# Optimization experiments

Measured on AMD Instinct MI355X. Metric: run time of the kernel, lower is better.

Reference implementation:

```python
import jax, jax.numpy as jnp
import numpy as np


def setup_inputs() -> dict:
    key = jax.random.key(0)
    b, l, d_model, n_head, topk = 2, 2048, 1024, 16, 32
    dh = d_model // n_head
    k0, k1, k2, k3, k4 = jax.random.split(key, 5)
    s = 1.0 / np.sqrt(d_model)
    return {
        "q_in": jax.random.normal(k0, (b, l, d_model), jnp.float32),
        "kv_in": jax.random.normal(k1, (b, l, d_model), jnp.float32),
        "w_q": jax.random.normal(k2, (d_model, d_model), jnp.float32) * s,
        "w_kv": jax.random.normal(k3, (d_model, 2 * dh), jnp.float32) * s,
        "w_concat": jax.random.normal(k4, (d_model, d_model), jnp.float32) * s,
        "topk": topk,
        "n_head": n_head,
    }


def _l2norm_seq(x):
    # F.normalize default dim=1 -> normalize along the sequence axis (faithful to source)
    n = jnp.sqrt(jnp.sum(x * x, axis=1, keepdims=True))
    return x / jnp.maximum(n, 1e-12)


def reference(q_in, kv_in, w_q, w_kv, w_concat, topk, n_head):
    b, l, d_model = q_in.shape
    dh = d_model // n_head
    scale = 1.0 / np.sqrt(dh)

    q = q_in @ w_q                                  # (b, l, d_model)
    kv = kv_in @ w_kv                               # (b, l, 2*dh)
    k, v = kv[..., :dh], kv[..., dh:]
    k, v = _l2norm_seq(k), _l2norm_seq(v)           # (b, l, dh) single shared KV head

    q = q.reshape(b, l, n_head, dh).transpose(0, 2, 1, 3)  # (b, h, l, dh)

    # one similarity matrix reused for local attention and kNN retrieval
    sims = jnp.einsum('bhld,bmd->bhlm', q, k)       # (b, h, l, m)

    # local SDPA (KV head broadcast over query heads)
    local = jnp.einsum('bhlm,bmd->bhld', jax.nn.softmax(sims * scale, axis=-1), v)

    # exact inner-product kNN over stored keys (faiss memory stores k only,
    # so retrieved key == retrieved value == nearest stored key vectors)
    _, idx = jax.lax.top_k(sims, topk)              # (b, h, l, topk)
    mem = jax.vmap(lambda kk, ii: kk[ii])(k, idx)   # (b, h, l, topk, dh)

    s_ret = jnp.einsum('bhld,bhltd->bhlt', q, mem) * scale
    retrieved = jnp.einsum('bhlt,bhltd->bhld', jax.nn.softmax(s_ret, axis=-1), mem)

    out = (local + retrieved).transpose(0, 2, 1, 3).reshape(b, l, d_model)
    return out @ w_concat
```

## Files before the change

kernel.cpp:

```cpp
#include <hip/hip_runtime.h>
#include <cstddef>
#include <cstring>

#define B_    2
#define L_    2048
#define DM_   1024
#define NH_   16
#define DH_   64
#define SCALE_ 0.125f

typedef __bf16 bf16x8 __attribute__((ext_vector_type(8)));
typedef float  f32x4  __attribute__((ext_vector_type(4)));
typedef unsigned short ushort8v __attribute__((ext_vector_type(8)));
typedef unsigned short ushort4v __attribute__((ext_vector_type(4)));
typedef unsigned long long u64;
typedef unsigned int u32;

__device__ __forceinline__ u32 flipf(float f) {
    u32 u = __float_as_uint(f);
    return (u & 0x80000000u) ? ~u : (u | 0x80000000u);
}
__device__ __forceinline__ float bf2f(unsigned short u) {
    return __uint_as_float(((u32)u) << 16);
}
__device__ __forceinline__ unsigned short f2bf(float f) {
    __bf16 h = (__bf16)f;
    unsigned short u;
    __builtin_memcpy(&u, &h, 2);
    return u;
}
__device__ __forceinline__ u32 flip16(unsigned short u) {
    return (u & 0x8000u) ? (u32)(~u & 0xffffu) : (u32)(u | 0x8000u);
}
__device__ __forceinline__ unsigned short unflip16(u32 k) {
    return (k & 0x8000u) ? (unsigned short)(k ^ 0x8000u) : (unsigned short)(~k & 0xffffu);
}

__global__ __launch_bounds__(256)
void wsplit3(const float* __restrict__ W, unsigned short* __restrict__ w1,
             unsigned short* __restrict__ w2, unsigned short* __restrict__ w3,
             int K, int N) {
    const int n0 = blockIdx.x << 6;
    const int k0 = blockIdx.y << 6;
    const int t  = threadIdx.x;
    __shared__ float s[64][65];
    const int rr = t >> 4;
    const int c4 = (t & 15) << 2;
    #pragma unroll
    for (int rep = 0; rep < 4; ++rep) {
        int k = rr + (rep << 4);
        float4 x = *(const float4*)(W + (size_t)(k0 + k) * N + n0 + c4);
        s[k][c4+0] = x.x; s[k][c4+1] = x.y; s[k][c4+2] = x.z; s[k][c4+3] = x.w;
    }
    __syncthreads();
    #pragma unroll
    for (int rep = 0; rep < 4; ++rep) {
        int n = rr + (rep << 4);
        ushort4v h, m, l;
        #pragma unroll
        for (int j = 0; j < 4; ++j) {
            float x = s[c4 + j][n];
            unsigned short hh = f2bf(x);
            float r = x - bf2f(hh);
            unsigned short mm = f2bf(r);
            float r2 = r - bf2f(mm);
            h[j] = hh; m[j] = mm; l[j] = f2bf(r2);
        }
        size_t o = (size_t)(n0 + n) * K + k0 + c4;
        *(ushort4v*)(w1 + o) = h;
        *(ushort4v*)(w2 + o) = m;
        *(ushort4v*)(w3 + o) = l;
    }
}

__global__ __launch_bounds__(256)
void asplit3(const float* __restrict__ X, unsigned short* __restrict__ p1,
             unsigned short* __restrict__ p2, unsigned short* __restrict__ p3) {
    const size_t i = ((size_t)blockIdx.x * 256 + threadIdx.x) * 8;
    float4 x0 = *(const float4*)(X + i);
    float4 x1 = *(const float4*)(X + i + 4);
    float xv[8] = {x0.x, x0.y, x0.z, x0.w, x1.x, x1.y, x1.z, x1.w};
    ushort8v h, m, l;
    #pragma unroll
    for (int e = 0; e < 8; ++e) {
        float x = xv[e];
        unsigned short hh = f2bf(x);
        float r = x - bf2f(hh);
        unsigned short mm = f2bf(r);
        h[e] = hh; m[e] = mm; l[e] = f2bf(r - bf2f(mm));
    }
    *(ushort8v*)(p1 + i) = h;
    *(ushort8v*)(p2 + i) = m;
    *(ushort8v*)(p3 + i) = l;
}

__global__ __launch_bounds__(256)
void asplit2(const float* __restrict__ X, unsigned short* __restrict__ p1,
             unsigned short* __restrict__ p2) {
    const size_t i = ((size_t)blockIdx.x * 256 + threadIdx.x) * 8;
    float4 x0 = *(const float4*)(X + i);
    float4 x1 = *(const float4*)(X + i + 4);
    float xv[8] = {x0.x, x0.y, x0.z, x0.w, x1.x, x1.y, x1.z, x1.w};
    ushort8v h, l;
    #pragma unroll
    for (int e = 0; e < 8; ++e) {
        float x = xv[e];
        unsigned short hh = f2bf(x);
        h[e] = hh; l[e] = f2bf(x - bf2f(hh));
    }
    *(ushort8v*)(p1 + i) = h;
    *(ushort8v*)(p2 + i) = l;
}

__global__ __launch_bounds__(256)
void gemm6p(const unsigned short* __restrict__ a1, const unsigned short* __restrict__ a2,
            const unsigned short* __restrict__ a3,
            const unsigned short* __restrict__ w1, const unsigned short* __restrict__ w2,
            const unsigned short* __restrict__ w3,
            float* __restrict__ C, int N, int K) {
    __shared__ __align__(16) unsigned short sA[3][128][40];
    __shared__ __align__(16) unsigned short sW[3][64][40];
    const int t    = threadIdx.x;
    const int wv   = t >> 6;
    const int lane = t & 63;
    const int quad = lane >> 4;
    const int n15  = lane & 15;
    const int bm = blockIdx.y << 7;
    const int bn = blockIdx.x << 6;
    const int wm = (wv >> 1) << 6;
    const int wn = (wv & 1) << 5;
    f32x4 acc[4][2];
    #pragma unroll
    for (int i = 0; i < 4; ++i)
        #pragma unroll
        for (int j = 0; j < 2; ++j)
            #pragma unroll
            for (int r = 0; r < 4; ++r) acc[i][j][r] = 0.f;

    const int ar  = t >> 1,  acg = (t & 1) << 4;
    const int wr  = t >> 2,  wcg = (t & 3) << 3;
    const size_t ao = (size_t)(bm + ar) * K + acg;
    const size_t wo = (size_t)(bn + wr) * K + wcg;

    for (int k0 = 0; k0 < K; k0 += 32) {
        ushort8v A1a = *(const ushort8v*)(a1 + ao + k0);
        ushort8v A1b = *(const ushort8v*)(a1 + ao + k0 + 8);
        ushort8v A2a = *(const ushort8v*)(a2 + ao + k0);
        ushort8v A2b = *(const ushort8v*)(a2 + ao + k0 + 8);
        ushort8v A3a = *(const ushort8v*)(a3 + ao + k0);
        ushort8v A3b = *(const ushort8v*)(a3 + ao + k0 + 8);
        ushort8v u1 = *(const ushort8v*)(w1 + wo + k0);
        ushort8v u2 = *(const ushort8v*)(w2 + wo + k0);
        ushort8v u3 = *(const ushort8v*)(w3 + wo + k0);
        __syncthreads();
        *(ushort8v*)&sA[0][ar][acg]     = A1a;
        *(ushort8v*)&sA[0][ar][acg + 8] = A1b;
        *(ushort8v*)&sA[1][ar][acg]     = A2a;
        *(ushort8v*)&sA[1][ar][acg + 8] = A2b;
        *(ushort8v*)&sA[2][ar][acg]     = A3a;
        *(ushort8v*)&sA[2][ar][acg + 8] = A3b;
        *(ushort8v*)&sW[0][wr][wcg] = u1;
        *(ushort8v*)&sW[1][wr][wcg] = u2;
        *(ushort8v*)&sW[2][wr][wcg] = u3;
        __syncthreads();
        bf16x8 af[3][4];
        #pragma unroll
        for (int mi = 0; mi < 4; ++mi) {
            af[0][mi] = *(const bf16x8*)&sA[0][wm + (mi << 4) + n15][quad << 3];
            af[1][mi] = *(const bf16x8*)&sA[1][wm + (mi << 4) + n15][quad << 3];
            af[2][mi] = *(const bf16x8*)&sA[2][wm + (mi << 4) + n15][quad << 3];
        }
        #pragma unroll
        for (int nj = 0; nj < 2; ++nj) {
            bf16x8 wf1 = *(const bf16x8*)&sW[0][wn + (nj << 4) + n15][quad << 3];
            bf16x8 wf2 = *(const bf16x8*)&sW[1][wn + (nj << 4) + n15][quad << 3];
            bf16x8 wf3 = *(const bf16x8*)&sW[2][wn + (nj << 4) + n15][quad << 3];
            #pragma unroll
            for (int mi = 0; mi < 4; ++mi) {
                acc[mi][nj] = __builtin_amdgcn_mfma_f32_16x16x32_bf16(af[0][mi], wf1, acc[mi][nj], 0, 0, 0);
                acc[mi][nj] = __builtin_amdgcn_mfma_f32_16x16x32_bf16(af[0][mi], wf2, acc[mi][nj], 0, 0, 0);
                acc[mi][nj] = __builtin_amdgcn_mfma_f32_16x16x32_bf16(af[1][mi], wf1, acc[mi][nj], 0, 0, 0);
                acc[mi][nj] = __builtin_amdgcn_mfma_f32_16x16x32_bf16(af[1][mi], wf2, acc[mi][nj], 0, 0, 0);
                acc[mi][nj] = __builtin_amdgcn_mfma_f32_16x16x32_bf16(af[0][mi], wf3, acc[mi][nj], 0, 0, 0);
                acc[mi][nj] = __builtin_amdgcn_mfma_f32_16x16x32_bf16(af[2][mi], wf1, acc[mi][nj], 0, 0, 0);
            }
        }
    }
    #pragma unroll
    for (int mi = 0; mi < 4; ++mi)
        #pragma unroll
        for (int nj = 0; nj < 2; ++nj)
            #pragma unroll
            for (int r = 0; r < 4; ++r)
                C[(size_t)(bm + wm + (mi << 4) + (quad << 2) + r) * N
                  + bn + wn + (nj << 4) + n15] = acc[mi][nj][r];
}

__global__ __launch_bounds__(256)
void gemm3p(const unsigned short* __restrict__ a1, const unsigned short* __restrict__ a2,
            const unsigned short* __restrict__ w1, const unsigned short* __restrict__ w2,
            float* __restrict__ C, int N, int K) {
    __shared__ __align__(16) unsigned short sA[2][128][40];
    __shared__ __align__(16) unsigned short sW[2][64][40];
    const int t    = threadIdx.x;
    const int wv   = t >> 6;
    const int lane = t & 63;
    const int quad = lane >> 4;
    const int n15  = lane & 15;
    const int bm = blockIdx.y << 7;
    const int bn = blockIdx.x << 6;
    const int wm = (wv >> 1) << 6;
    const int wn = (wv & 1) << 5;
    f32x4 acc[4][2];
    #pragma unroll
    for (int i = 0; i < 4; ++i)
        #pragma unroll
        for (int j = 0; j < 2; ++j)
            #pragma unroll
            for (int r = 0; r < 4; ++r) acc[i][j][r] = 0.f;

    const int ar  = t >> 1,  acg = (t & 1) << 4;
    const int wr  = t >> 2,  wcg = (t & 3) << 3;
    const size_t ao = (size_t)(bm + ar) * K + acg;
    const size_t wo = (size_t)(bn + wr) * K + wcg;

    for (int k0 = 0; k0 < K; k0 += 32) {
        ushort8v A1a = *(const ushort8v*)(a1 + ao + k0);
        ushort8v A1b = *(const ushort8v*)(a1 + ao + k0 + 8);
        ushort8v A2a = *(const ushort8v*)(a2 + ao + k0);
        ushort8v A2b = *(const ushort8v*)(a2 + ao + k0 + 8);
        ushort8v u1 = *(const ushort8v*)(w1 + wo + k0);
        ushort8v u2 = *(const ushort8v*)(w2 + wo + k0);
        __syncthreads();
        *(ushort8v*)&sA[0][ar][acg]     = A1a;
        *(ushort8v*)&sA[0][ar][acg + 8] = A1b;
        *(ushort8v*)&sA[1][ar][acg]     = A2a;
        *(ushort8v*)&sA[1][ar][acg + 8] = A2b;
        *(ushort8v*)&sW[0][wr][wcg] = u1;
        *(ushort8v*)&sW[1][wr][wcg] = u2;
        __syncthreads();
        bf16x8 af[2][4];
        #pragma unroll
        for (int mi = 0; mi < 4; ++mi) {
            af[0][mi] = *(const bf16x8*)&sA[0][wm + (mi << 4) + n15][quad << 3];
            af[1][mi] = *(const bf16x8*)&sA[1][wm + (mi << 4) + n15][quad << 3];
        }
        #pragma unroll
        for (int nj = 0; nj < 2; ++nj) {
            bf16x8 wf1 = *(const bf16x8*)&sW[0][wn + (nj << 4) + n15][quad << 3];
            bf16x8 wf2 = *(const bf16x8*)&sW[1][wn + (nj << 4) + n15][quad << 3];
            #pragma unroll
            for (int mi = 0; mi < 4; ++mi) {
                acc[mi][nj] = __builtin_amdgcn_mfma_f32_16x16x32_bf16(af[0][mi], wf1, acc[mi][nj], 0, 0, 0);
                acc[mi][nj] = __builtin_amdgcn_mfma_f32_16x16x32_bf16(af[0][mi], wf2, acc[mi][nj], 0, 0, 0);
                acc[mi][nj] = __builtin_amdgcn_mfma_f32_16x16x32_bf16(af[1][mi], wf1, acc[mi][nj], 0, 0, 0);
            }
        }
    }
    #pragma unroll
    for (int mi = 0; mi < 4; ++mi)
        #pragma unroll
        for (int nj = 0; nj < 2; ++nj)
            #pragma unroll
            for (int r = 0; r < 4; ++r)
                C[(size_t)(bm + wm + (mi << 4) + (quad << 2) + r) * N
                  + bn + wn + (nj << 4) + n15] = acc[mi][nj][r];
}

__global__ __launch_bounds__(256)
void col_norms(const float* __restrict__ kv, float* __restrict__ invn) {
    const int bc = blockIdx.x;
    const int b  = bc >> 7;
    const int c  = bc & 127;
    const int t  = threadIdx.x;
    const float* base = kv + (size_t)b * L_ * 128 + c;
    float ss = 0.f;
    for (int l = t; l < L_; l += 256) {
        float x = base[(size_t)l * 128];
        ss += x * x;
    }
    #pragma unroll
    for (int off = 32; off; off >>= 1) ss += __shfl_xor(ss, off);
    __shared__ float red[4];
    if ((t & 63) == 0) red[t >> 6] = ss;
    __syncthreads();
    if (t == 0) {
        float tot = red[0] + red[1] + red[2] + red[3];
        invn[bc] = 1.f / fmaxf(sqrtf(tot), 1e-12f);
    }
}

__global__ __launch_bounds__(256)
void scale_kv(const float* __restrict__ kv, const float* __restrict__ invn,
              float* __restrict__ kn, __bf16* __restrict__ kh,
              __bf16* __restrict__ vT) {
    const int b  = blockIdx.y;
    const int l0 = blockIdx.x << 6;
    const int t  = threadIdx.x;
    __shared__ float s_inv[128];
    __shared__ float s_vt[64][65];
    if (t < 128) s_inv[t] = invn[b * 128 + t];
    __syncthreads();
    #pragma unroll
    for (int rep = 0; rep < 8; ++rep) {
        int idx = (rep << 8) + t;
        int li  = idx >> 5;
        int c4  = (idx & 31) << 2;
        float4 x = *(const float4*)(kv + ((size_t)(b * L_ + l0 + li)) * 128 + c4);
        x.x *= s_inv[c4]; x.y *= s_inv[c4+1]; x.z *= s_inv[c4+2]; x.w *= s_inv[c4+3];
        if (c4 < 64) {
            size_t o = ((size_t)(b * L_ + l0 + li)) * DH_ + c4;
            *(float4*)(kn + o) = x;
            kh[o+0] = (__bf16)x.x; kh[o+1] = (__bf16)x.y;
            kh[o+2] = (__bf16)x.z; kh[o+3] = (__bf16)x.w;
        } else {
            int d = c4 - 64;
            s_vt[d+0][li] = x.x; s_vt[d+1][li] = x.y; s_vt[d+2][li] = x.z; s_vt[d+3][li] = x.w;
        }
    }
    __syncthreads();
    #pragma unroll
    for (int rep = 0; rep < 4; ++rep) {
        int idx = (rep << 8) + t;
        int d   = idx >> 4;
        int j   = (idx & 15) << 2;
        size_t o = ((size_t)b * DH_ + d) * L_ + l0 + j;
        vT[o+0] = (__bf16)s_vt[d][j+0];
        vT[o+1] = (__bf16)s_vt[d][j+1];
        vT[o+2] = (__bf16)s_vt[d][j+2];
        vT[o+3] = (__bf16)s_vt[d][j+3];
    }
}

__global__ __launch_bounds__(256, 4)
void attn_part(const float* __restrict__ q,
               const __bf16* __restrict__ kh,
               const __bf16* __restrict__ vT,
               float* __restrict__ attn,
               u32* __restrict__ cand,
               int* __restrict__ candC) {
    const int tile = blockIdx.x;
    const int h    = blockIdx.y;
    const int b    = blockIdx.z;
    const int l0   = tile << 4;
    const int t    = threadIdx.x;
    const int w    = t >> 6;
    const int lane = t & 63;
    const int quad = lane >> 4;
    const int n15  = lane & 15;

    __shared__ __align__(16) union SMem {
        unsigned short sims[16 * 1024];
        struct { float local[16][66]; float denom[16]; } fin;
    } sm;
    __shared__ u32 s_prov[16][96];
    unsigned short* s_sims = sm.sims;
    const int swz = n15 & 7;

    bf16x8 qf[2];
    {
        const float* qp = q + ((size_t)(b * L_ + l0 + n15)) * DM_ + h * DH_ + (quad << 3);
        #pragma unroll
        for (int ks = 0; ks < 2; ++ks) {
            float4 x0 = *(const float4*)(qp + (ks << 5));
            float4 x1 = *(const float4*)(qp + (ks << 5) + 4);
            float xv[8] = {x0.x, x0.y, x0.z, x0.w, x1.x, x1.y, x1.z, x1.w};
            #pragma unroll
            for (int i2 = 0; i2 < 8; ++i2) qf[ks][i2] = (__bf16)xv[i2];
        }
    }

    f32x4 accL[4] = {{0,0,0,0},{0,0,0,0},{0,0,0,0},{0,0,0,0}};
    float psum = 0.f;
    float bvmax[4] = {-3e38f, -3e38f, -3e38f, -3e38f};
    int   c0[4]    = {0, 0, 0, 0};
    const __bf16* khb = kh + (size_t)b * L_ * DH_;
    const __bf16* vtb = vT + (size_t)b * DH_ * L_;
    const int rg0 = ((b * NH_ + h) * L_) + l0;

    #pragma unroll 1
    for (int hf = 0; hf < 2; ++hf) {
        #pragma unroll
        for (int g = 0; g < 4; ++g) {
            bf16x8 kf[8];
            const __bf16* kp = khb + (size_t)((hf << 10) + (w << 8) + (g << 6) + n15) * DH_ + (quad << 3);
            #pragma unroll
            for (int jj = 0; jj < 4; ++jj) {
                kf[2*jj]   = *(const bf16x8*)(kp + (size_t)(jj << 4) * DH_);
                kf[2*jj+1] = *(const bf16x8*)(kp + (size_t)(jj << 4) * DH_ + 32);
            }
            #pragma unroll
            for (int jj = 0; jj < 4; ++jj) {
                int m0 = (w << 8) + (g << 6) + (jj << 4);
                f32x4 acc = {0.f, 0.f, 0.f, 0.f};
                acc = __builtin_amdgcn_mfma_f32_16x16x32_bf16(kf[2*jj],   qf[0], acc, 0, 0, 0);
                acc = __builtin_amdgcn_mfma_f32_16x16x32_bf16(kf[2*jj+1], qf[1], acc, 0, 0, 0);
                u32 lo = (u32)f2bf(acc[0]) | ((u32)f2bf(acc[1]) << 16);
                u32 hi = (u32)f2bf(acc[2]) | ((u32)f2bf(acc[3]) << 16);
                u64 pk = ((u64)hi << 32) | lo;
                int lb = (m0 << 1) + (quad << 3);
                int pb = ((lb & ~15) ^ (swz << 4)) | (lb & 15);
                *(u64*)((char*)s_sims + (n15 << 11) + pb) = pk;
            }
        }
        __syncthreads();

        #pragma unroll 1
        for (int rr2 = 0; rr2 < 4; ++rr2) {
            const int r = (w << 2) + rr2;
            const unsigned short* srow = s_sims + (r << 10);
            ushort8v rv[2];
            rv[0] = *(const ushort8v*)(srow + (lane << 3));
            rv[1] = *(const ushort8v*)(srow + 512 + (lane << 3));
            const int lx = (lane ^ (r & 7)) << 3;
            float bv = -3e38f;
            #pragma unroll
            for (int j = 0; j < 2; ++j)
                #pragma unroll
                for (int e = 0; e < 8; ++e) bv = fmaxf(bv, bf2f(rv[j][e]));
            bvmax[rr2] = fmaxf(bvmax[rr2], bv);
            if (hf == 0) {
                u32 key = flip16(f2bf(bv));
                u32 thr = 0;
                #pragma unroll
                for (int bp = 15; bp >= 0; --bp) {
                    u32 tt = thr | (1u << bp);
                    if (__popcll(__ballot(key >= tt)) >= 32) thr = tt;
                }
                float thrv = bf2f(unflip16(thr)) - 0.01f;
                int base = 0;
                #pragma unroll
                for (int j = 0; j < 2; ++j) {
                    #pragma unroll
                    for (int e = 0; e < 8; ++e) {
                        bool pred = bf2f(rv[j][e]) >= thrv;
                        u64 mk = __ballot(pred);
                        if (pred) {
                            int pos = base + __popcll(mk & ((1ull << lane) - 1));
                            if (pos < 96)
                                s_prov[r][pos] = ((u32)rv[j][e] << 16)
                                               | (u32)((j << 9) + lx + e);
                        }
                        base += __popcll(mk);
                    }
                }
                c0[rr2] = base < 96 ? base : 96;
            } else {
                u32 key = flip16(f2bf(bvmax[rr2]));
                u32 thr = 0;
                #pragma unroll
                for (int bp = 15; bp >= 0; --bp) {
                    u32 tt = thr | (1u << bp);
                    if (__popcll(__ballot(key >= tt)) >= 32) thr = tt;
                }
                float thrv = bf2f(unflip16(thr)) - 0.01f;
                const int cc0 = c0[rr2];
                u32 e0 = (lane < cc0) ? s_prov[r][lane] : 0u;
                u32 e1 = (64 + lane < cc0) ? s_prov[r][64 + lane] : 0u;
                u32* cr = cand + (size_t)(rg0 + r) * 96;
                int base = 0;
                {
                    bool pred = (lane < cc0)
                              && (bf2f((unsigned short)(e0 >> 16)) >= thrv);
                    u64 mk = __ballot(pred);
                    if (pred) {
                        int pos = __popcll(mk & ((1ull << lane) - 1));
                        cr[pos] = e0;
                    }
                    base = __popcll(mk);
                }
                if (cc0 > 64) {
                    bool pred = (64 + lane < cc0)
                              && (bf2f((unsigned short)(e1 >> 16)) >= thrv);
                    u64 mk = __ballot(pred);
                    if (pred) {
                        int pos = base + __popcll(mk & ((1ull << lane) - 1));
                        if (pos < 96) cr[pos] = e1;
                    }
                    base += __popcll(mk);
                }
                #pragma unroll
                for (int j = 0; j < 2; ++j) {
                    #pragma unroll
                    for (int e = 0; e < 8; ++e) {
                        bool pred = bf2f(rv[j][e]) >= thrv;
                        u64 mk = __ballot(pred);
                        if (pred) {
                            int pos = base + __popcll(mk & ((1ull << lane) - 1));
                            if (pos < 96)
                                cr[pos] = ((u32)rv[j][e] << 16)
                                        | (u32)(1024 + (j << 9) + lx + e);
                        }
                        base += __popcll(mk);
                    }
                }
                if (lane == 0) candC[rg0 + r] = base < 96 ? base : 96;
            }
        }

        #pragma unroll
        for (int g = 0; g < 4; ++g) {
            bf16x8 bvv[2][4];
            #pragma unroll
            for (int t2 = 0; t2 < 2; ++t2)
                #pragma unroll
                for (int nn = 0; nn < 4; ++nn)
                    bvv[t2][nn] = *(const bf16x8*)(vtb + (size_t)((nn << 4) + n15) * L_
                                  + (hf << 10) + (w << 8) + (g << 6) + (t2 << 5) + (quad << 3));
            #pragma unroll
            for (int t2 = 0; t2 < 2; ++t2) {
                int mb = (w << 8) + (g << 6) + (t2 << 5);
                int unit = (mb >> 3) + quad;
                ushort8v pu = *(const ushort8v*)(s_sims + (n15 << 10) + ((unit ^ swz) << 3));
                bf16x8 af;
                #pragma unroll
                for (int e = 0; e < 8; ++e) {
                    float p = __expf(SCALE_ * bf2f(pu[e]));
                    psum += p;
                    af[e] = (__bf16)p;
                }
                #pragma unroll
                for (int nn = 0; nn < 4; ++nn)
                    accL[nn] = __builtin_amdgcn_mfma_f32_16x16x32_bf16(af, bvv[t2][nn], accL[nn], 0, 0, 0);
            }
        }
        __syncthreads();
    }

    {
        float* sl = &sm.fin.local[0][0];
        #pragma unroll 1
        for (int i = t; i < 16 * 66 + 16; i += 256) sl[i] = 0.f;
    }
    __syncthreads();

    psum += __shfl_xor(psum, 16);
    psum += __shfl_xor(psum, 32);
    if (lane < 16) atomicAdd(&sm.fin.denom[lane], psum);
    #pragma unroll
    for (int nn = 0; nn < 4; ++nn)
        #pragma unroll
        for (int rr = 0; rr < 4; ++rr)
            atomicAdd(&sm.fin.local[(quad << 2) + rr][(nn << 4) + n15], accL[nn][rr]);
    __syncthreads();

    {
        int r  = t >> 4;
        int d0 = (t & 15) << 2;
        float inv = 1.f / sm.fin.denom[r];
        float* op = attn + ((size_t)(b * L_ + l0 + r)) * DM_ + h * DH_ + d0;
        op[0] = sm.fin.local[r][d0+0] * inv;
        op[1] = sm.fin.local[r][d0+1] * inv;
        op[2] = sm.fin.local[r][d0+2] * inv;
        op[3] = sm.fin.local[r][d0+3] * inv;
    }
}

__global__ __launch_bounds__(256)
void topk_merge(const float* __restrict__ q, const float* __restrict__ kn,
                const u32* __restrict__ cand, const int* __restrict__ candC,
                float* __restrict__ attn) {
    const int wv   = threadIdx.x >> 6;
    const int lane = threadIdx.x & 63;
    const int row  = (blockIdx.x << 2) + wv;
    const int l = row & (L_ - 1);
    const int h = (row >> 11) & (NH_ - 1);
    const int b = row >> 15;
    __shared__ float s_dot[4][96];
    __shared__ __align__(16) u64 s_sel[4][32];

    const int C = candC[row];
    const u32* cr = cand + (size_t)row * 96;
    const float* knb = kn + (size_t)b * L_ * DH_;
    const float* qr  = q + ((size_t)(b * L_ + l)) * DM_ + h * DH_;

    int mreg0 = (lane < C) ? (int)(cr[lane] & 0xffffu) : 0;
    int mreg1 = (64 + lane < C) ? (int)(cr[64 + lane] & 0xffffu) : 0;

    const int cg = lane >> 4;
    const int dg = lane & 15;
    float4 qx = *(const float4*)(qr + (dg << 2));

    #pragma unroll 2
    for (int base = 0; base < C; base += 4) {
        int ci = base + cg;
        int src = ci & 63;
        int mA = __shfl(mreg0, src);
        int mB = __shfl(mreg1, src);
        int m  = (ci < 64) ? mA : mB;
        float4 kx = *(const float4*)(knb + (size_t)m * DH_ + (dg << 2));
        float p = kx.x * qx.x + kx.y * qx.y + kx.z * qx.z + kx.w * qx.w;
        p += __shfl_xor(p, 1);
        p += __shfl_xor(p, 2);
        p += __shfl_xor(p, 4);
        p += __shfl_xor(p, 8);
        if (dg == 0 && ci < C) s_dot[wv][ci] = p;
    }

    float dotA = (lane < C) ? s_dot[wv][lane] : 0.f;
    float dotB = (64 + lane < C) ? s_dot[wv][64 + lane] : 0.f;
    u32 keyA = (lane < C) ? flipf(dotA) : 0u;
    u32 keyB = (64 + lane < C) ? flipf(dotB) : 0u;

    u32 thr2 = 0;
    if (C <= 64) {
        #pragma unroll
        for (int bp = 31; bp >= 0; --bp) {
            u32 tt = thr2 | (1u << bp);
            if (__popcll(__ballot(keyA >= tt)) >= 32) thr2 = tt;
        }
    } else {
        #pragma unroll
        for (int bp = 31; bp >= 0; --bp) {
            u32 tt = thr2 | (1u << bp);
            int c2 = __popcll(__ballot(keyA >= tt)) + __popcll(__ballot(keyB >= tt));
            if (c2 >= 32) thr2 = tt;
        }
    }
    {
        bool pA = keyA >= thr2;
        u64 mkA = __ballot(pA);
        if (pA) {
            int pos = __popcll(mkA & ((1ull << lane) - 1));
            if (pos < 32) {
                float pt = __expf(SCALE_ * dotA);
                s_sel[wv][pos] = ((u64)__float_as_uint(pt) << 32) | (u32)mreg0;
            }
        }
        if (C > 64) {
            int cA = __popcll(mkA);
            bool pB = keyB >= thr2;
            u64 mkB = __ballot(pB);
            if (pB) {
                int pos = cA + __popcll(mkB & ((1ull << lane) - 1));
                if (pos < 32) {
                    float pt = __expf(SCALE_ * dotB);
                    s_sel[wv][pos] = ((u64)__float_as_uint(pt) << 32) | (u32)mreg1;
                }
            }
        }
    }
    {
        float pts[32];
        int   ms[32];
        #pragma unroll
        for (int i = 0; i < 32; ++i) {
            u64 s0 = s_sel[wv][i];
            pts[i] = __uint_as_float((u32)(s0 >> 32));
            ms[i]  = (int)(u32)(s0 & 0xffffffffu);
        }
        const float* knb2 = knb + lane;
        float kvv[32];
        #pragma unroll
        for (int i = 0; i < 32; ++i) kvv[i] = knb2[(size_t)ms[i] * DH_];
        float rs = 0.f, ret = 0.f;
        #pragma unroll
        for (int i = 0; i < 16; ++i) {
            rs  += pts[2*i] + pts[2*i+1];
            ret += pts[2*i] * kvv[2*i] + pts[2*i+1] * kvv[2*i+1];
        }
        size_t oa = ((size_t)(b * L_ + l)) * DM_ + h * DH_ + lane;
        attn[oa] = attn[oa] + ret / rs;
    }
}

extern "C" void kernel_launch(void* const* d_in, const int* in_sizes, int n_in,
                              void* d_out, int out_size, void* d_ws, size_t ws_size,
                              hipStream_t stream) {
    const float* q_in     = (const float*)d_in[0];
    const float* kv_in    = (const float*)d_in[1];
    const float* w_q      = (const float*)d_in[2];
    const float* w_kv     = (const float*)d_in[3];
    const float* w_concat = (const float*)d_in[4];
    float* out = (float*)d_out;

    float* ws   = (float*)d_ws;
    float* q    = ws;
    float* attn = ws + 4194304;
    float* kv   = attn;
    float* kn   = ws + 8388608;
    float* invn = ws + 8650752;
    unsigned short* us = (unsigned short*)(ws + 8651008);
    unsigned short* kh_u = us;
    unsigned short* vT_u = us + 262144;
    unsigned short* wq1  = us + 524288;
    unsigned short* wq2  = wq1 + 1048576;
    unsigned short* wq3  = wq2 + 1048576;
    unsigned short* wc1  = wq3 + 1048576;
    unsigned short* wc2  = wc1 + 1048576;
    unsigned short* wkv1 = wc2 + 1048576;
    unsigned short* wkv2 = wkv1 + 131072;
    unsigned short* wkv3 = wkv2 + 131072;
    u32* cand = (u32*)(wkv3 + 131072);
    int* candC = (int*)(cand + 65536 * 96);
    __bf16* kh = (__bf16*)kh_u;
    __bf16* vT = (__bf16*)vT_u;

    unsigned short* r1 = (unsigned short*)cand;
    unsigned short* ap1 = r1;
    unsigned short* ap2 = r1 + 4194304;
    unsigned short* ap3 = r1 + 8388608;
    unsigned short* wc3 = ap1;

    wsplit3<<<dim3(DM_ / 64, DM_ / 64), 256, 0, stream>>>(w_q, wq1, wq2, wq3, DM_, DM_);
    wsplit3<<<dim3(DM_ / 64, DM_ / 64), 256, 0, stream>>>(w_concat, wc1, wc2, wc3, DM_, DM_);
    wsplit3<<<dim3(128 / 64, DM_ / 64), 256, 0, stream>>>(w_kv, wkv1, wkv2, wkv3, DM_, 128);

    asplit3<<<(B_ * L_ * DM_) / 2048, 256, 0, stream>>>(q_in, ap1, ap2, ap3);
    gemm6p<<<dim3(DM_ / 64, (B_ * L_) / 128), 256, 0, stream>>>(ap1, ap2, ap3, wq1, wq2, wq3, q, DM_, DM_);

    asplit3<<<(B_ * L_ * DM_) / 2048, 256, 0, stream>>>(kv_in, ap1, ap2, ap3);
    gemm6p<<<dim3(128 / 64, (B_ * L_) / 128), 256, 0, stream>>>(ap1, ap2, ap3, wkv1, wkv2, wkv3, kv, 128, DM_);

    col_norms<<<B_ * 128, 256, 0, stream>>>(kv, invn);
    scale_kv<<<dim3(L_ / 64, B_), 256, 0, stream>>>(kv, invn, kn, kh, vT);

    attn_part<<<dim3(L_ / 16, NH_, B_), 256, 0, stream>>>(q, kh, vT, attn, cand, candC);
    topk_merge<<<(B_ * NH_ * L_) / 4, 256, 0, stream>>>(q, kn, cand, candC, attn);

    asplit2<<<(B_ * L_ * DM_) / 2048, 256, 0, stream>>>(attn, ap1, ap2);
    gemm3p<<<dim3(DM_ / 64, (B_ * L_) / 128), 256, 0, stream>>>(ap1, ap2, wc1, wc2, out, DM_, DM_);
}
```

Baseline: 709.5 us.

## Process key sequence in four 512-wide chunks to halve sims LDS buffer

Splits the key loop in the attention kernel from two 1024-wide halves into four 512-wide chunks, so the per-block bf16 similarity buffer in LDS shrinks to half its size. Top-k candidate filtering is restructured into an incremental pass that recompacts the shared candidate list on every chunk and writes to global memory only on the last one. This lowers LDS use per block to allow more resident blocks, at the cost of extra barriers, ballot-threshold passes and candidate recompaction work per chunk.

```diff
diff --git a/kernel.cpp b/kernel.cpp
--- a/kernel.cpp
+++ b/kernel.cpp
@@ -350,7 +350,7 @@
     const int n15  = lane & 15;
 
     __shared__ __align__(16) union SMem {
-        unsigned short sims[16 * 1024];
+        unsigned short sims[16 * 512];
         struct { float local[16][66]; float denom[16]; } fin;
     } sm;
     __shared__ u32 s_prov[16][96];
@@ -379,11 +379,11 @@
     const int rg0 = ((b * NH_ + h) * L_) + l0;
 
     #pragma unroll 1
-    for (int hf = 0; hf < 2; ++hf) {
-        #pragma unroll
-        for (int g = 0; g < 4; ++g) {
+    for (int ck = 0; ck < 4; ++ck) {
+        #pragma unroll
+        for (int g = 0; g < 2; ++g) {
             bf16x8 kf[8];
-            const __bf16* kp = khb + (size_t)((hf << 10) + (w << 8) + (g << 6) + n15) * DH_ + (quad << 3);
+            const __bf16* kp = khb + (size_t)((ck << 9) + (w << 7) + (g << 6) + n15) * DH_ + (quad << 3);
             #pragma unroll
             for (int jj = 0; jj < 4; ++jj) {
                 kf[2*jj]   = *(const bf16x8*)(kp + (size_t)(jj << 4) * DH_);
@@ -391,7 +391,7 @@
             }
             #pragma unroll
             for (int jj = 0; jj < 4; ++jj) {
-                int m0 = (w << 8) + (g << 6) + (jj << 4);
+                int m0 = (w << 7) + (g << 6) + (jj << 4);
                 f32x4 acc = {0.f, 0.f, 0.f, 0.f};
                 acc = __builtin_amdgcn_mfma_f32_16x16x32_bf16(kf[2*jj],   qf[0], acc, 0, 0, 0);
                 acc = __builtin_amdgcn_mfma_f32_16x16x32_bf16(kf[2*jj+1], qf[1], acc, 0, 0, 0);
@@ -400,7 +400,7 @@
                 u64 pk = ((u64)hi << 32) | lo;
                 int lb = (m0 << 1) + (quad << 3);
                 int pb = ((lb & ~15) ^ (swz << 4)) | (lb & 15);
-                *(u64*)((char*)s_sims + (n15 << 11) + pb) = pk;
+                *(u64*)((char*)s_sims + (n15 << 10) + pb) = pk;
             }
         }
         __syncthreads();
@@ -408,52 +408,73 @@
         #pragma unroll 1
         for (int rr2 = 0; rr2 < 4; ++rr2) {
             const int r = (w << 2) + rr2;
-            const unsigned short* srow = s_sims + (r << 10);
-            ushort8v rv[2];
-            rv[0] = *(const ushort8v*)(srow + (lane << 3));
-            rv[1] = *(const ushort8v*)(srow + 512 + (lane << 3));
+            ushort8v rv = *(const ushort8v*)(s_sims + (r << 9) + (lane << 3));
             const int lx = (lane ^ (r & 7)) << 3;
             float bv = -3e38f;
             #pragma unroll
-            for (int j = 0; j < 2; ++j)
-                #pragma unroll
-                for (int e = 0; e < 8; ++e) bv = fmaxf(bv, bf2f(rv[j][e]));
+            for (int e = 0; e < 8; ++e) bv = fmaxf(bv, bf2f(rv[e]));
             bvmax[rr2] = fmaxf(bvmax[rr2], bv);
-            if (hf == 0) {
-                u32 key = flip16(f2bf(bv));
-                u32 thr = 0;
-                #pragma unroll
-                for (int bp = 15; bp >= 0; --bp) {
-                    u32 tt = thr | (1u << bp);
-                    if (__popcll(__ballot(key >= tt)) >= 32) thr = tt;
-                }
-                float thrv = bf2f(unflip16(thr)) - 0.01f;
+            u32 key = flip16(f2bf(bvmax[rr2]));
+            u32 thr = 0;
+            #pragma unroll
+            for (int bp = 15; bp >= 0; --bp) {
+                u32 tt = thr | (1u << bp);
+                if (__popcll(__ballot(key >= tt)) >= 32) thr = tt;
+            }
+            float thrv = bf2f(unflip16(thr)) - 0.01f;
+            if (ck == 0) {
                 int base = 0;
                 #pragma unroll
-                for (int j = 0; j < 2; ++j) {
-                    #pragma unroll
-                    for (int e = 0; e < 8; ++e) {
-                        bool pred = bf2f(rv[j][e]) >= thrv;
-                        u64 mk = __ballot(pred);
-                        if (pred) {
-                            int pos = base + __popcll(mk & ((1ull << lane) - 1));
-                            if (pos < 96)
-                                s_prov[r][pos] = ((u32)rv[j][e] << 16)
-                                               | (u32)((j << 9) + lx + e);
-                        }
-                        base += __popcll(mk);
+                for (int e = 0; e < 8; ++e) {
+                    bool pred = bf2f(rv[e]) >= thrv;
+                    u64 mk = __ballot(pred);
+                    if (pred) {
+                        int pos = base + __popcll(mk & ((1ull << lane) - 1));
+                        if (pos < 96)
+                            s_prov[r][pos] = ((u32)rv[e] << 16) | (u32)(lx + e);
                     }
+                    base += __popcll(mk);
+                }
+                c0[rr2] = base < 96 ? base : 96;
+            } else if (ck < 3) {
+                const int cc0 = c0[rr2];
+                u32 e0 = (lane < cc0) ? s_prov[r][lane] : 0u;
+                u32 e1 = (64 + lane < cc0) ? s_prov[r][64 + lane] : 0u;
+                int base = 0;
+                {
+                    bool pred = (lane < cc0)
+                              && (bf2f((unsigned short)(e0 >> 16)) >= thrv);
+                    u64 mk = __ballot(pred);
+                    if (pred) {
+                        int pos = __popcll(mk & ((1ull << lane) - 1));
+                        s_prov[r][pos] = e0;
+                    }
+                    base = __popcll(mk);
+                }
+                if (cc0 > 64) {
+                    bool pred = (64 + lane < cc0)
+                              && (bf2f((unsigned short)(e1 >> 16)) >= thrv);
+                    u64 mk = __ballot(pred);
+                    if (pred) {
+                        int pos = base + __popcll(mk & ((1ull << lane) - 1));
+                        if (pos < 96) s_prov[r][pos] = e1;
+                    }
+                    base += __popcll(mk);
+                }
+                #pragma unroll
+                for (int e = 0; e < 8; ++e) {
+                    bool pred = bf2f(rv[e]) >= thrv;
+                    u64 mk = __ballot(pred);
+                    if (pred) {
+                        int pos = base + __popcll(mk & ((1ull << lane) - 1));
+                        if (pos < 96)
+                            s_prov[r][pos] = ((u32)rv[e] << 16)
+                                           | (u32)((ck << 9) + lx + e);
+                    }
+                    base += __popcll(mk);
                 }
                 c0[rr2] = base < 96 ? base : 96;
             } else {
-                u32 key = flip16(f2bf(bvmax[rr2]));
-                u32 thr = 0;
-                #pragma unroll
-                for (int bp = 15; bp >= 0; --bp) {
-                    u32 tt = thr | (1u << bp);
-                    if (__popcll(__ballot(key >= tt)) >= 32) thr = tt;
-                }
-                float thrv = bf2f(unflip16(thr)) - 0.01f;
                 const int cc0 = c0[rr2];
                 u32 e0 = (lane < cc0) ? s_prov[r][lane] : 0u;
                 u32 e1 = (64 + lane < cc0) ? s_prov[r][64 + lane] : 0u;
@@ -480,38 +501,35 @@
                     base += __popcll(mk);
                 }
                 #pragma unroll
-                for (int j = 0; j < 2; ++j) {
-                    #pragma unroll
-                    for (int e = 0; e < 8; ++e) {
-                        bool pred = bf2f(rv[j][e]) >= thrv;
-                        u64 mk = __ballot(pred);
-                        if (pred) {
-                            int pos = base + __popcll(mk & ((1ull << lane) - 1));
-                            if (pos < 96)
-                                cr[pos] = ((u32)rv[j][e] << 16)
-                                        | (u32)(1024 + (j << 9) + lx + e);
-                        }
-                        base += __popcll(mk);
+                for (int e = 0; e < 8; ++e) {
+                    bool pred = bf2f(rv[e]) >= thrv;
+                    u64 mk = __ballot(pred);
+                    if (pred) {
+                        int pos = base + __popcll(mk & ((1ull << lane) - 1));
+                        if (pos < 96)
+                            cr[pos] = ((u32)rv[e] << 16)
+                                    | (u32)((3 << 9) + lx + e);
                     }
+                    base += __popcll(mk);
                 }
                 if (lane == 0) candC[rg0 + r] = base < 96 ? base : 96;
             }
         }
 
         #pragma unroll
-        for (int g = 0; g < 4; ++g) {
+        for (int g = 0; g < 2; ++g) {
             bf16x8 bvv[2][4];
             #pragma unroll
             for (int t2 = 0; t2 < 2; ++t2)
                 #pragma unroll
                 for (int nn = 0; nn < 4; ++nn)
                     bvv[t2][nn] = *(const bf16x8*)(vtb + (size_t)((nn << 4) + n15) * L_
-                                  + (hf << 10) + (w << 8) + (g << 6) + (t2 << 5) + (quad << 3));
+                                  + (ck << 9) + (w << 7) + (g << 6) + (t2 << 5) + (quad << 3));
             #pragma unroll
             for (int t2 = 0; t2 < 2; ++t2) {
-                int mb = (w << 8) + (g << 6) + (t2 << 5);
+                int mb = (w << 7) + (g << 6) + (t2 << 5);
                 int unit = (mb >> 3) + quad;
-                ushort8v pu = *(const ushort8v*)(s_sims + (n15 << 10) + ((unit ^ swz) << 3));
+                ushort8v pu = *(const ushort8v*)(s_sims + (n15 << 9) + ((unit ^ swz) << 3));
                 bf16x8 af;
                 #pragma unroll
                 for (int e = 0; e < 8; ++e) {
```

Result: slower. 734.1 us (+3.5%).

## Fuse top-k candidate refinement into attention kernel, drop candidate buffers

Applied to the files above, without the earlier changes.

Moves the exact top-k refinement and retrieved-value accumulation from a separate topk_merge kernel into the end of the attention kernel. Candidates stay in shared memory (s_prov) and the retrieved result is added to the local output before a single store. This removes the global candidate write/read round trip, one kernel launch, and the read-modify-write of attn. In exchange the attention kernel does more serial per-row work and uses more shared memory, which may lower occupancy.

```diff
diff --git a/kernel.cpp b/kernel.cpp
--- a/kernel.cpp
+++ b/kernel.cpp
@@ -333,12 +333,11 @@
 }
 
 __global__ __launch_bounds__(256, 4)
-void attn_part(const float* __restrict__ q,
-               const __bf16* __restrict__ kh,
-               const __bf16* __restrict__ vT,
-               float* __restrict__ attn,
-               u32* __restrict__ cand,
-               int* __restrict__ candC) {
+void attn_fused(const float* __restrict__ q,
+                const __bf16* __restrict__ kh,
+                const __bf16* __restrict__ vT,
+                const float* __restrict__ kn,
+                float* __restrict__ attn) {
     const int tile = blockIdx.x;
     const int h    = blockIdx.y;
     const int b    = blockIdx.z;
@@ -351,7 +350,13 @@
 
     __shared__ __align__(16) union SMem {
         unsigned short sims[16 * 1024];
-        struct { float local[16][66]; float denom[16]; } fin;
+        struct {
+            float local[16][66];
+            float denom[16];
+            float dot[16][96];
+            float ret[16][64];
+            u64   sel[16][32];
+        } fin;
     } sm;
     __shared__ u32 s_prov[16][96];
     unsigned short* s_sims = sm.sims;
@@ -376,7 +381,7 @@
     int   c0[4]    = {0, 0, 0, 0};
     const __bf16* khb = kh + (size_t)b * L_ * DH_;
     const __bf16* vtb = vT + (size_t)b * DH_ * L_;
-    const int rg0 = ((b * NH_ + h) * L_) + l0;
+    const float*  knb = kn + (size_t)b * L_ * DH_;
 
     #pragma unroll 1
     for (int hf = 0; hf < 2; ++hf) {
@@ -457,7 +462,6 @@
                 const int cc0 = c0[rr2];
                 u32 e0 = (lane < cc0) ? s_prov[r][lane] : 0u;
                 u32 e1 = (64 + lane < cc0) ? s_prov[r][64 + lane] : 0u;
-                u32* cr = cand + (size_t)(rg0 + r) * 96;
                 int base = 0;
                 {
                     bool pred = (lane < cc0)
@@ -465,7 +469,7 @@
                     u64 mk = __ballot(pred);
                     if (pred) {
                         int pos = __popcll(mk & ((1ull << lane) - 1));
-                        cr[pos] = e0;
+                        s_prov[r][pos] = e0;
                     }
                     base = __popcll(mk);
                 }
@@ -475,7 +479,7 @@
                     u64 mk = __ballot(pred);
                     if (pred) {
                         int pos = base + __popcll(mk & ((1ull << lane) - 1));
-                        if (pos < 96) cr[pos] = e1;
+                        if (pos < 96) s_prov[r][pos] = e1;
                     }
                     base += __popcll(mk);
                 }
@@ -488,13 +492,13 @@
                         if (pred) {
                             int pos = base + __popcll(mk & ((1ull << lane) - 1));
                             if (pos < 96)
-                                cr[pos] = ((u32)rv[j][e] << 16)
-                                        | (u32)(1024 + (j << 9) + lx + e);
+                                s_prov[r][pos] = ((u32)rv[j][e] << 16)
+                                               | (u32)(1024 + (j << 9) + lx + e);
                         }
                         base += __popcll(mk);
                     }
                 }
-                if (lane == 0) candC[rg0 + r] = base < 96 ? base : 96;
+                c0[rr2] = base < 96 ? base : 96;
             }
         }
 
@@ -542,6 +546,91 @@
         #pragma unroll
         for (int rr = 0; rr < 4; ++rr)
             atomicAdd(&sm.fin.local[(quad << 2) + rr][(nn << 4) + n15], accL[nn][rr]);
+
+    {
+        const int cg = lane >> 4;
+        const int dg = lane & 15;
+        #pragma unroll 1
+        for (int rr2 = 0; rr2 < 4; ++rr2) {
+            const int r = (w << 2) + rr2;
+            const int C = c0[rr2];
+            const float* qr = q + ((size_t)(b * L_ + l0 + r)) * DM_ + h * DH_;
+            float4 qx = *(const float4*)(qr + (dg << 2));
+            #pragma unroll 2
+            for (int base = 0; base < C; base += 4) {
+                int ci = base + cg;
+                int m = (ci < C) ? (int)(s_prov[r][ci] & 0xffffu) : 0;
+                float4 kx = *(const float4*)(knb + (size_t)m * DH_ + (dg << 2));
+                float p = kx.x * qx.x + kx.y * qx.y + kx.z * qx.z + kx.w * qx.w;
+                p += __shfl_xor(p, 1);
+                p += __shfl_xor(p, 2);
+                p += __shfl_xor(p, 4);
+                p += __shfl_xor(p, 8);
+                if (dg == 0 && ci < C) sm.fin.dot[r][ci] = p;
+            }
+            int m0r = (lane < C) ? (int)(s_prov[r][lane] & 0xffffu) : 0;
+            int m1r = (64 + lane < C) ? (int)(s_prov[r][64 + lane] & 0xffffu) : 0;
+            float dotA = (lane < C) ? sm.fin.dot[r][lane] : 0.f;
+            float dotB = (64 + lane < C) ? sm.fin.dot[r][64 + lane] : 0.f;
+            u32 keyA = (lane < C) ? flipf(dotA) : 0u;
+            u32 keyB = (64 + lane < C) ? flipf(dotB) : 0u;
+            u32 thr2 = 0;
+            if (C <= 64) {
+                #pragma unroll
+                for (int bp = 31; bp >= 0; --bp) {
+                    u32 tt = thr2 | (1u << bp);
+                    if (__popcll(__ballot(keyA >= tt)) >= 32) thr2 = tt;
+                }
+            } else {
+                #pragma unroll
+                for (int bp = 31; bp >= 0; --bp) {
+                    u32 tt = thr2 | (1u << bp);
+                    int c2 = __popcll(__ballot(keyA >= tt)) + __popcll(__ballot(keyB >= tt));
+                    if (c2 >= 32) thr2 = tt;
+                }
+            }
+            {
+                bool pA = keyA >= thr2;
+                u64 mkA = __ballot(pA);
+                if (pA) {
+                    int pos = __popcll(mkA & ((1ull << lane) - 1));
+                    if (pos < 32) {
+                        float pt = __expf(SCALE_ * dotA);
+                        sm.fin.sel[r][pos] = ((u64)__float_as_uint(pt) << 32) | (u32)m0r;
+                    }
+                }
+                if (C > 64) {
+                    int cA = __popcll(mkA);
+                    bool pB = keyB >= thr2;
+                    u64 mkB = __ballot(pB);
+                    if (pB) {
+                        int pos = cA + __popcll(mkB & ((1ull << lane) - 1));
+                        if (pos < 32) {
+                            float pt = __expf(SCALE_ * dotB);
+                            sm.fin.sel[r][pos] = ((u64)__float_as_uint(pt) << 32) | (u32)m1r;
+                        }
+                    }
+                }
+            }
+            float rs = 0.f, ret = 0.f;
+            const float* knl = knb + lane;
+            #pragma unroll
+            for (int c2 = 0; c2 < 2; ++c2) {
+                float pts[16]; int ms[16]; float kvv[16];
+                #pragma unroll
+                for (int i = 0; i < 16; ++i) {
+                    u64 s0 = sm.fin.sel[r][(c2 << 4) + i];
+                    pts[i] = __uint_as_float((u32)(s0 >> 32));
+                    ms[i]  = (int)(u32)(s0 & 0xffffffffu);
+                }
+                #pragma unroll
+                for (int i = 0; i < 16; ++i) kvv[i] = knl[(size_t)ms[i] * DH_];
+                #pragma unroll
+                for (int i = 0; i < 16; ++i) { rs += pts[i]; ret += pts[i] * kvv[i]; }
+            }
+            sm.fin.ret[r][lane] = ret / rs;
+        }
+    }
     __syncthreads();
 
     {
@@ -549,118 +638,10 @@
         int d0 = (t & 15) << 2;
         float inv = 1.f / sm.fin.denom[r];
         float* op = attn + ((size_t)(b * L_ + l0 + r)) * DM_ + h * DH_ + d0;
-        op[0] = sm.fin.local[r][d0+0] * inv;
-        op[1] = sm.fin.local[r][d0+1] * inv;
-        op[2] = sm.fin.local[r][d0+2] * inv;
-        op[3] = sm.fin.local[r][d0+3] * inv;
-    }
-}
-
-__global__ __launch_bounds__(256)
-void topk_merge(const float* __restrict__ q, const float* __restrict__ kn,
-                const u32* __restrict__ cand, const int* __restrict__ candC,
-                float* __restrict__ attn) {
-    const int wv   = threadIdx.x >> 6;
-    const int lane = threadIdx.x & 63;
-    const int row  = (blockIdx.x << 2) + wv;
-    const int l = row & (L_ - 1);
-    const int h = (row >> 11) & (NH_ - 1);
-    const int b = row >> 15;
-    __shared__ float s_dot[4][96];
-    __shared__ __align__(16) u64 s_sel[4][32];
-
-    const int C = candC[row];
-    const u32* cr = cand + (size_t)row * 96;
-    const float* knb = kn + (size_t)b * L_ * DH_;
-    const float* qr  = q + ((size_t)(b * L_ + l)) * DM_ + h * DH_;
-
-    int mreg0 = (lane < C) ? (int)(cr[lane] & 0xffffu) : 0;
-    int mreg1 = (64 + lane < C) ? (int)(cr[64 + lane] & 0xffffu) : 0;
-
-    const int cg = lane >> 4;
-    const int dg = lane & 15;
-    float4 qx = *(const float4*)(qr + (dg << 2));
-
-    #pragma unroll 2
-    for (int base = 0; base < C; base += 4) {
-        int ci = base + cg;
-        int src = ci & 63;
-        int mA = __shfl(mreg0, src);
-        int mB = __shfl(mreg1, src);
-        int m  = (ci < 64) ? mA : mB;
-        float4 kx = *(const float4*)(knb + (size_t)m * DH_ + (dg << 2));
-        float p = kx.x * qx.x + kx.y * qx.y + kx.z * qx.z + kx.w * qx.w;
-        p += __shfl_xor(p, 1);
-        p += __shfl_xor(p, 2);
-        p += __shfl_xor(p, 4);
-        p += __shfl_xor(p, 8);
-        if (dg == 0 && ci < C) s_dot[wv][ci] = p;
-    }
-
-    float dotA = (lane < C) ? s_dot[wv][lane] : 0.f;
-    float dotB = (64 + lane < C) ? s_dot[wv][64 + lane] : 0.f;
-    u32 keyA = (lane < C) ? flipf(dotA) : 0u;
-    u32 keyB = (64 + lane < C) ? flipf(dotB) : 0u;
-
-    u32 thr2 = 0;
-    if (C <= 64) {
-        #pragma unroll
-        for (int bp = 31; bp >= 0; --bp) {
-            u32 tt = thr2 | (1u << bp);
-            if (__popcll(__ballot(keyA >= tt)) >= 32) thr2 = tt;
-        }
-    } else {
-        #pragma unroll
-        for (int bp = 31; bp >= 0; --bp) {
-            u32 tt = thr2 | (1u << bp);
-            int c2 = __popcll(__ballot(keyA >= tt)) + __popcll(__ballot(keyB >= tt));
-            if (c2 >= 32) thr2 = tt;
-        }
-    }
-    {
-        bool pA = keyA >= thr2;
-        u64 mkA = __ballot(pA);
-        if (pA) {
-            int pos = __popcll(mkA & ((1ull << lane) - 1));
-            if (pos < 32) {
-                float pt = __expf(SCALE_ * dotA);
-                s_sel[wv][pos] = ((u64)__float_as_uint(pt) << 32) | (u32)mreg0;
-            }
-        }
-        if (C > 64) {
-            int cA = __popcll(mkA);
-            bool pB = keyB >= thr2;
-            u64 mkB = __ballot(pB);
-            if (pB) {
-                int pos = cA + __popcll(mkB & ((1ull << lane) - 1));
-                if (pos < 32) {
-                    float pt = __expf(SCALE_ * dotB);
-                    s_sel[wv][pos] = ((u64)__float_as_uint(pt) << 32) | (u32)mreg1;
-                }
-            }
-        }
-    }
-    {
-        float pts[32];
-        int   ms[32];
-        #pragma unroll
-        for (int i = 0; i < 32; ++i) {
-            u64 s0 = s_sel[wv][i];
-            pts[i] = __uint_as_float((u32)(s0 >> 32));
-            ms[i]  = (int)(u32)(s0 & 0xffffffffu);
-        }
-        const float* knb2 = knb + lane;
-        float kvv[32];
-        #pragma unroll
-        for (int i = 0; i < 32; ++i) kvv[i] = knb2[(size_t)ms[i] * DH_];
-        float rs = 0.f, ret = 0.f;
-        #pragma unroll
-        for (int i = 0; i < 16; ++i) {
-            rs  += pts[2*i] + pts[2*i+1];
-            ret += pts[2*i] * kvv[2*i] + pts[2*i+1] * kvv[2*i+1];
-        }
-        size_t oa = ((size_t)(b * L_ + l)) * DM_ + h * DH_ + lane;
-        attn[oa] = attn[oa] + ret / rs;
+        op[0] = sm.fin.local[r][d0+0] * inv + sm.fin.ret[r][d0+0];
+        op[1] = sm.fin.local[r][d0+1] * inv + sm.fin.ret[r][d0+1];
+        op[2] = sm.fin.local[r][d0+2] * inv + sm.fin.ret[r][d0+2];
+        op[3] = sm.fin.local[r][d0+3] * inv + sm.fin.ret[r][d0+3];
     }
 }
 
@@ -691,12 +672,10 @@
     unsigned short* wkv1 = wc2 + 1048576;
     unsigned short* wkv2 = wkv1 + 131072;
     unsigned short* wkv3 = wkv2 + 131072;
-    u32* cand = (u32*)(wkv3 + 131072);
-    int* candC = (int*)(cand + 65536 * 96);
     __bf16* kh = (__bf16*)kh_u;
     __bf16* vT = (__bf16*)vT_u;
 
-    unsigned short* r1 = (unsigned short*)cand;
+    unsigned short* r1 = wkv3 + 131072;
     unsigned short* ap1 = r1;
     unsigned short* ap2 = r1 + 4194304;
     unsigned short* ap3 = r1 + 8388608;
@@ -715,8 +694,7 @@
     col_norms<<<B_ * 128, 256, 0, stream>>>(kv, invn);
     scale_kv<<<dim3(L_ / 64, B_), 256, 0, stream>>>(kv, invn, kn, kh, vT);
 
-    attn_part<<<dim3(L_ / 16, NH_, B_), 256, 0, stream>>>(q, kh, vT, attn, cand, candC);
-    topk_merge<<<(B_ * NH_ * L_) / 4, 256, 0, stream>>>(q, kn, cand, candC, attn);
+    attn_fused<<<dim3(L_ / 16, NH_, B_), 256, 0, stream>>>(q, kh, vT, kn, attn);
 
     asplit2<<<(B_ * L_ * DM_) / 2048, 256, 0, stream>>>(attn, ap1, ap2);
     gemm3p<<<dim3(DM_ / 64, (B_ * L_) / 128), 256, 0, stream>>>(ap1, ap2, wc1, wc2, out, DM_, DM_);
```

Result: faster. 694.2 us (-2.2%).
